# Kernel tuning notes

Hardware: AMD Instinct MI355X
Metric: run time of the kernel (lower is better)

The kernel has to match this reference:

```python
import jax, jax.numpy as jnp
import numpy as np

C = 20        # class_num
B = 2         # boxes per cell, N = B*5 + C = 30
S = 7         # grid size
NB = 16384    # batch
LAMBDA_COORD = 5.0
LAMBDA_NOOBJ = 0.5
OBJ_P = 0.2


def setup_inputs() -> dict:
    key = jax.random.key(0)
    ks = jax.random.split(key, 8)
    pred = jax.random.uniform(ks[0], (NB, S, S, B * 5 + C), jnp.float32)
    # object indicator per cell (target conf channel must be exactly 1 for obj cells)
    obj = (jax.random.uniform(ks[1], (NB, S, S, 1)) < OBJ_P).astype(jnp.float32)
    parts = []
    for b in range(B):
        xy = jax.random.uniform(ks[2 + 2 * b], (NB, S, S, 2), jnp.float32)
        wh = jax.random.uniform(ks[3 + 2 * b], (NB, S, S, 2), jnp.float32) * 0.9 + 0.05
        parts += [xy, wh, obj]
    cls = jax.random.uniform(ks[6], (NB, S, S, C), jnp.float32)
    target = jnp.concatenate(parts + [cls], axis=-1)
    return {"pred_tensor": pred, "target_tensor": target}


def _yolo_loss(pred, target):
    Nb, Sg, _, N = pred.shape
    Bb = (N - C) // 5
    dt = pred.dtype
    # grid[..., 0] = column (x offset), grid[..., 1] = row (y offset)
    gx, gy = jnp.meshgrid(jnp.arange(Sg), jnp.arange(Sg), indexing="xy")
    grid = jnp.stack([gx, gy], axis=-1).astype(dt)          # [S,S,2]

    pb = pred[..., : 5 * Bb].reshape(Nb, Sg, Sg, Bb, 5)      # raw pred boxes [Nb,S,S,B,5]
    tb0 = target[..., :5]                                    # raw gt box 0  [Nb,S,S,5]

    # txty -> absolute xy (normalized by S); wh stays raw
    pxy = (pb[..., :2] + grid[None, :, :, None, :]) / Sg
    pwh = pb[..., 2:4]
    gxy = (tb0[..., :2] + grid[None]) / Sg
    gwh = tb0[..., 2:4]

    # corners
    p1, p2 = pxy - 0.5 * pwh, pxy + 0.5 * pwh                # [Nb,S,S,B,2]
    g1 = (gxy - 0.5 * gwh)[..., None, :]                     # [Nb,S,S,1,2]
    g2 = (gxy + 0.5 * gwh)[..., None, :]

    # IoU of gt box against each of the B pred boxes, per cell
    wh = jnp.clip(jnp.minimum(g2, p2) - jnp.maximum(g1, p1), 0.0)
    inter = wh[..., 0] * wh[..., 1]                          # [Nb,S,S,B]
    area_p = pwh[..., 0] * pwh[..., 1]
    area_g = (gwh[..., 0] * gwh[..., 1])[..., None]
    iou = inter / (area_g + area_p - inter)

    best = jnp.argmax(iou, axis=-1)                          # [Nb,S,S]
    best_iou = jax.lax.stop_gradient(jnp.max(iou, axis=-1))  # .item() in torch detaches
    best_box = jnp.take_along_axis(pb, best[..., None, None], axis=3)[..., 0, :]  # raw [Nb,S,S,5]

    obj = target[..., 4] == 1.0
    objf = obj.astype(dt)
    noobjf = (target[..., 4] < 1.0).astype(dt)

    # coord losses (responsible box only)
    loss_xy = LAMBDA_COORD * jnp.sum(objf[..., None] * (best_box[..., :2] - tb0[..., :2]) ** 2)
    gwh_safe = jnp.where(obj[..., None], gwh, 1.0)           # keep sqrt grads finite under mask
    pwh_safe = jnp.where(obj[..., None], jnp.clip(best_box[..., 2:4], 0.0, 1.0), 1.0)
    loss_wh = LAMBDA_COORD * jnp.sum(objf[..., None] * (jnp.sqrt(pwh_safe) - jnp.sqrt(gwh_safe)) ** 2)

    loss_conf_posi = jnp.sum(objf * (best_box[..., 4] - best_iou) ** 2)
    loss_class = jnp.sum(objf[..., None] * (pred[..., 5 * Bb:] - target[..., 5 * Bb:]) ** 2)

    # negative conf: all B confs in no-obj cells + non-best confs in obj cells
    conf_all = pb[..., 4]                                    # [Nb,S,S,B]
    onehot = jax.nn.one_hot(best, Bb, dtype=dt)
    neg_w = objf[..., None] * (1.0 - onehot) + noobjf[..., None]
    loss_conf_nega = LAMBDA_NOOBJ * jnp.sum(neg_w * conf_all ** 2)

    total = loss_xy + loss_wh + loss_conf_posi + loss_conf_nega + loss_class
    bs = jnp.asarray(Nb, dt)
    return total / bs / bs  # original divides by batch_size twice


def reference(pred_tensor, target_tensor):
    return _yolo_loss(pred_tensor, target_tensor)
```

## Files before the change

kernel.cpp:

```cpp
#include <hip/hip_runtime.h>
#include <math.h>

constexpr int NCH = 30;
constexpr int CPB = 256;
constexpr int NT  = 256;
constexpr int NCHK = CPB * NCH / 4;
constexpr int SPP = 11;
constexpr int STP = 6;

__global__ __launch_bounds__(NT) void yolo_loss_main(
    const float* __restrict__ pred, const float* __restrict__ targ,
    float* __restrict__ partial, int ncells)
{
  __shared__ float sp_box[CPB * SPP];
  __shared__ float st_box[CPB * STP];
  __shared__ float scp[NCHK];
  __shared__ float swred[NT / 64];

  const int tid = threadIdx.x;
  const int cell0 = blockIdx.x * CPB;
  const int nc = min(CPB, ncells - cell0);
  const size_t base = (size_t)cell0 * NCH;

  float sum = 0.0f;

  if (nc == CPB) {
    const float4* gp = (const float4*)(pred + base);
    const float4* gt = (const float4*)(targ + base);
    for (int f = tid; f < NCHK; f += NT) {
      float4 pv = gp[f];
      float4 tv = gt[f];
      int d0 = 4 * f;
      int cell = d0 / NCH;
      int ch0 = d0 - cell * NCH;
      float cp = 0.0f;
      #pragma unroll
      for (int j = 0; j < 4; ++j) {
        int ch = ch0 + j;
        int c = cell;
        if (ch >= NCH) { ch -= NCH; c += 1; }
        float pd = ((const float*)&pv)[j];
        float td = ((const float*)&tv)[j];
        if (ch >= 10) {
          float dd = pd - td;
          cp += dd * dd;
        } else {
          sp_box[c * SPP + ch] = pd;
          if (ch < 5) st_box[c * STP + ch] = td;
        }
      }
      scp[f] = cp;
    }
  } else {
    for (int i = tid; i < NCHK; i += NT) scp[i] = 0.0f;
    for (int i = tid; i < nc; i += NT) {
      const float* p = pred + base + (size_t)i * NCH;
      const float* t = targ + base + (size_t)i * NCH;
      for (int k = 0; k < 10; ++k) sp_box[i * SPP + k] = p[k];
      for (int k = 0; k < 5;  ++k) st_box[i * STP + k] = t[k];
      float o = (t[4] == 1.0f) ? 1.0f : 0.0f;
      for (int k = 10; k < NCH; ++k) {
        float dd = p[k] - t[k];
        sum += o * dd * dd;
      }
    }
  }
  __syncthreads();

  if (tid < nc) {
    const float* p = sp_box + tid * SPP;
    const float* t = st_box + tid * STP;
    int cellg = cell0 + tid;
    int rem = cellg % 49;
    int row = rem / 7;
    float fi = (float)row;
    float fj = (float)(rem - row * 7);

    float tx = t[0], ty = t[1], tw = t[2], th = t[3];
    bool obj = (t[4] == 1.0f);

    if (obj) {
      int m = tid >> 1;
      const float* cpp = scp + 15 * m;
      float cl;
      if ((tid & 1) == 0)
        cl = cpp[2] + cpp[3] + cpp[4] + cpp[5] + cpp[6] + cpp[7];
      else
        cl = cpp[10] + cpp[11] + cpp[12] + cpp[13] + cpp[14];
      sum += cl;
    }

    float gx = (tx + fj) / 7.0f;
    float gy = (ty + fi) / 7.0f;
    float g1x = gx - 0.5f * tw, g1y = gy - 0.5f * th;
    float g2x = gx + 0.5f * tw, g2y = gy + 0.5f * th;
    float area_g = tw * th;

    float px0 = p[0], py0 = p[1], pw0 = p[2], ph0 = p[3], pc0 = p[4];
    float px1 = p[5], py1 = p[6], pw1 = p[7], ph1 = p[8], pc1 = p[9];

    float iou0, iou1;
    {
      float cx = (px0 + fj) / 7.0f, cy = (py0 + fi) / 7.0f;
      float wx = fminf(g2x, cx + 0.5f * pw0) - fmaxf(g1x, cx - 0.5f * pw0);
      float wy = fminf(g2y, cy + 0.5f * ph0) - fmaxf(g1y, cy - 0.5f * ph0);
      wx = fmaxf(wx, 0.0f); wy = fmaxf(wy, 0.0f);
      float inter = wx * wy;
      iou0 = inter / (area_g + pw0 * ph0 - inter);
    }
    {
      float cx = (px1 + fj) / 7.0f, cy = (py1 + fi) / 7.0f;
      float wx = fminf(g2x, cx + 0.5f * pw1) - fmaxf(g1x, cx - 0.5f * pw1);
      float wy = fminf(g2y, cy + 0.5f * ph1) - fmaxf(g1y, cy - 0.5f * ph1);
      wx = fmaxf(wx, 0.0f); wy = fmaxf(wy, 0.0f);
      float inter = wx * wy;
      iou1 = inter / (area_g + pw1 * ph1 - inter);
    }

    bool b1 = (iou1 > iou0);
    float biou = fmaxf(iou0, iou1);

    float lneg = 0.0f;
    if (!obj || b1)  lneg += pc0 * pc0;
    if (!obj || !b1) lneg += pc1 * pc1;
    sum += 0.5f * lneg;

    if (obj) {
      float bx = b1 ? px1 : px0;
      float by = b1 ? py1 : py0;
      float bw = b1 ? pw1 : pw0;
      float bh = b1 ? ph1 : ph0;
      float bc = b1 ? pc1 : pc0;
      float dx = bx - tx, dy = by - ty;
      sum += 5.0f * (dx * dx + dy * dy);
      float cw  = fminf(fmaxf(bw, 0.0f), 1.0f);
      float chh = fminf(fmaxf(bh, 0.0f), 1.0f);
      float sw_ = sqrtf(cw)  - sqrtf(tw);
      float sh_ = sqrtf(chh) - sqrtf(th);
      sum += 5.0f * (sw_ * sw_ + sh_ * sh_);
      float dc = bc - biou;
      sum += dc * dc;
    }
  }

  #pragma unroll
  for (int off = 32; off > 0; off >>= 1) sum += __shfl_down(sum, off);
  if ((tid & 63) == 0) swred[tid >> 6] = sum;
  __syncthreads();
  if (tid == 0) {
    float s = 0.0f;
    #pragma unroll
    for (int w = 0; w < NT / 64; ++w) s += swred[w];
    partial[blockIdx.x] = s;
  }
}

__global__ __launch_bounds__(256) void yolo_loss_reduce(
    const float* __restrict__ partial, int n, float* __restrict__ out,
    float scale)
{
  __shared__ float swred[4];
  float s = 0.0f;
  for (int i = threadIdx.x; i < n; i += 256) s += partial[i];
  #pragma unroll
  for (int off = 32; off > 0; off >>= 1) s += __shfl_down(s, off);
  if ((threadIdx.x & 63) == 0) swred[threadIdx.x >> 6] = s;
  __syncthreads();
  if (threadIdx.x == 0)
    out[0] = (swred[0] + swred[1] + swred[2] + swred[3]) * scale;
}

extern "C" void kernel_launch(void* const* d_in, const int* in_sizes, int n_in,
                              void* d_out, int out_size, void* d_ws, size_t ws_size,
                              hipStream_t stream) {
  const float* pred = (const float*)d_in[0];
  const float* targ = (const float*)d_in[1];
  float* out = (float*)d_out;
  float* partial = (float*)d_ws;

  int total = in_sizes[0];
  int ncells = total / NCH;
  int nb = ncells / 49;
  int blocks = (ncells + CPB - 1) / CPB;
  float scale = 1.0f / ((float)nb * (float)nb);

  yolo_loss_main<<<blocks, NT, 0, stream>>>(pred, targ, partial, ncells);
  yolo_loss_reduce<<<1, 256, 0, stream>>>(partial, blocks, out, scale);
}
```

Baseline: 42.05 us.

## Stage box fields as float4 in LDS and batch global loads per thread

Moves to 320 threads so the 1920 float4 chunks of a 256-cell tile split evenly into six per thread. The chunks are loaded in two unrolled batches of three pred and three target float4s to raise memory-level parallelism. Box fields go into shared memory as whole float4 chunks arranged by cell pair instead of scattered scalar stores, and the compute phase reads them back with float4 LDS loads. This cuts LDS store count and branch divergence but adds register pressure, and 64 of the 320 threads sit idle during the per-cell compute phase.

```diff
diff --git a/kernel.cpp b/kernel.cpp
--- a/kernel.cpp
+++ b/kernel.cpp
@@ -1,21 +1,21 @@
 #include <hip/hip_runtime.h>
 #include <math.h>
 
-constexpr int NCH = 30;
-constexpr int CPB = 256;
-constexpr int NT  = 256;
+constexpr int NCH  = 30;
+constexpr int CPB  = 256;
+constexpr int NT   = 320;
 constexpr int NCHK = CPB * NCH / 4;
-constexpr int SPP = 11;
-constexpr int STP = 6;
+constexpr int NIT  = NCHK / NT;
+
 
 __global__ __launch_bounds__(NT) void yolo_loss_main(
     const float* __restrict__ pred, const float* __restrict__ targ,
     float* __restrict__ partial, int ncells)
 {
-  __shared__ float sp_box[CPB * SPP];
-  __shared__ float st_box[CPB * STP];
-  __shared__ float scp[NCHK];
-  __shared__ float swred[NT / 64];
+  __shared__ float4 sp4[(CPB / 2) * 6];
+  __shared__ float4 st4[(CPB / 2) * 4];
+  __shared__ float  scp[NCHK];
+  __shared__ float  swred[NT / 64];
 
   const int tid = threadIdx.x;
   const int cell0 = blockIdx.x * CPB;
@@ -27,77 +27,120 @@
   if (nc == CPB) {
     const float4* gp = (const float4*)(pred + base);
     const float4* gt = (const float4*)(targ + base);
-    for (int f = tid; f < NCHK; f += NT) {
-      float4 pv = gp[f];
-      float4 tv = gt[f];
-      int d0 = 4 * f;
-      int cell = d0 / NCH;
-      int ch0 = d0 - cell * NCH;
-      float cp = 0.0f;
+
+    #pragma unroll
+    for (int b = 0; b < 2; ++b) {
+      float4 pv[3], tv[3];
       #pragma unroll
-      for (int j = 0; j < 4; ++j) {
-        int ch = ch0 + j;
-        int c = cell;
-        if (ch >= NCH) { ch -= NCH; c += 1; }
-        float pd = ((const float*)&pv)[j];
-        float td = ((const float*)&tv)[j];
-        if (ch >= 10) {
-          float dd = pd - td;
-          cp += dd * dd;
-        } else {
-          sp_box[c * SPP + ch] = pd;
-          if (ch < 5) st_box[c * STP + ch] = td;
+      for (int i = 0; i < 3; ++i) pv[i] = gp[(3 * b + i) * NT + tid];
+      #pragma unroll
+      for (int i = 0; i < 3; ++i) tv[i] = gt[(3 * b + i) * NT + tid];
+
+      #pragma unroll
+      for (int i = 0; i < 3; ++i) {
+        int f = (3 * b + i) * NT + tid;
+        int m = f / 15;
+        int k = f - m * 15;
+        int ch0 = 4 * k - (k >= 8 ? 30 : 0);
+
+        float cp = 0.0f;
+        #pragma unroll
+        for (int j = 0; j < 4; ++j) {
+          int ch = ch0 + j;
+          bool cls = (ch >= 10) & (ch < 30);
+          float d = ((const float*)&pv[i])[j] - ((const float*)&tv[i])[j];
+          cp += cls ? d * d : 0.0f;
+        }
+        scp[f] = cp;
+
+        if (k < 3 || (k >= 7 && k <= 9)) {
+          int ps = (k < 3) ? k : (k - 4);
+          sp4[m * 6 + ps] = pv[i];
+        }
+        if (k < 2 || k == 7 || k == 8) {
+          int ts = (k < 2) ? k : (k - 5);
+          st4[m * 4 + ts] = tv[i];
         }
       }
-      scp[f] = cp;
     }
   } else {
     for (int i = tid; i < NCHK; i += NT) scp[i] = 0.0f;
+    float* spf = (float*)sp4;
+    float* stf = (float*)st4;
     for (int i = tid; i < nc; i += NT) {
       const float* p = pred + base + (size_t)i * NCH;
       const float* t = targ + base + (size_t)i * NCH;
-      for (int k = 0; k < 10; ++k) sp_box[i * SPP + k] = p[k];
-      for (int k = 0; k < 5;  ++k) st_box[i * STP + k] = t[k];
+      int m = i >> 1;
+      if ((i & 1) == 0) {
+        for (int q = 0; q < 8; ++q) spf[(m * 6 + 0) * 4 + q] = p[q];
+        spf[(m * 6 + 2) * 4 + 0] = p[8];
+        spf[(m * 6 + 2) * 4 + 1] = p[9];
+        for (int q = 0; q < 4; ++q) stf[(m * 4 + 0) * 4 + q] = t[q];
+        stf[(m * 4 + 1) * 4 + 0] = t[4];
+      } else {
+        spf[(m * 6 + 3) * 4 + 2] = p[0];
+        spf[(m * 6 + 3) * 4 + 3] = p[1];
+        for (int q = 0; q < 8; ++q) spf[(m * 6 + 4) * 4 + q] = p[2 + q];
+        stf[(m * 4 + 2) * 4 + 2] = t[0];
+        stf[(m * 4 + 2) * 4 + 3] = t[1];
+        stf[(m * 4 + 3) * 4 + 0] = t[2];
+        stf[(m * 4 + 3) * 4 + 1] = t[3];
+        stf[(m * 4 + 3) * 4 + 2] = t[4];
+      }
       float o = (t[4] == 1.0f) ? 1.0f : 0.0f;
-      for (int k = 10; k < NCH; ++k) {
-        float dd = p[k] - t[k];
-        sum += o * dd * dd;
-      }
+      float cs = 0.0f;
+      for (int q = 10; q < NCH; ++q) { float d = p[q] - t[q]; cs += d * d; }
+      sum += o * cs;
     }
   }
   __syncthreads();
 
   if (tid < nc) {
-    const float* p = sp_box + tid * SPP;
-    const float* t = st_box + tid * STP;
+    int m = tid >> 1;
+    bool odd = tid & 1;
+    float4 A = sp4[m * 6 + (odd ? 3 : 0)];
+    float4 B = sp4[m * 6 + (odd ? 4 : 1)];
+    float4 Cc = sp4[m * 6 + (odd ? 5 : 2)];
+    float px0, py0, pw0, ph0, pc0, px1, py1, pw1, ph1, pc1;
+    float tx, ty, tw, th, tobj;
+    if (!odd) {
+      px0 = A.x;  py0 = A.y;  pw0 = A.z;  ph0 = A.w;
+      pc0 = B.x;  px1 = B.y;  py1 = B.z;  pw1 = B.w;
+      ph1 = Cc.x; pc1 = Cc.y;
+      float4 T0 = st4[m * 4 + 0];
+      tx = T0.x; ty = T0.y; tw = T0.z; th = T0.w;
+      tobj = st4[m * 4 + 1].x;
+    } else {
+      px0 = A.z;  py0 = A.w;
+      pw0 = B.x;  ph0 = B.y;  pc0 = B.z;  px1 = B.w;
+      py1 = Cc.x; pw1 = Cc.y; ph1 = Cc.z; pc1 = Cc.w;
+      float4 T2 = st4[m * 4 + 2];
+      float4 T3 = st4[m * 4 + 3];
+      tx = T2.z; ty = T2.w; tw = T3.x; th = T3.y; tobj = T3.z;
+    }
+    bool obj = (tobj == 1.0f);
+
+    if (obj) {
+      const float* cpp = scp + 15 * m;
+      float cl;
+      if (!odd)
+        cl = cpp[2] + cpp[3] + cpp[4] + cpp[5] + cpp[6] + cpp[7];
+      else
+        cl = cpp[10] + cpp[11] + cpp[12] + cpp[13] + cpp[14];
+      sum += cl;
+    }
+
     int cellg = cell0 + tid;
     int rem = cellg % 49;
     int row = rem / 7;
     float fi = (float)row;
     float fj = (float)(rem - row * 7);
 
-    float tx = t[0], ty = t[1], tw = t[2], th = t[3];
-    bool obj = (t[4] == 1.0f);
-
-    if (obj) {
-      int m = tid >> 1;
-      const float* cpp = scp + 15 * m;
-      float cl;
-      if ((tid & 1) == 0)
-        cl = cpp[2] + cpp[3] + cpp[4] + cpp[5] + cpp[6] + cpp[7];
-      else
-        cl = cpp[10] + cpp[11] + cpp[12] + cpp[13] + cpp[14];
-      sum += cl;
-    }
-
     float gx = (tx + fj) / 7.0f;
     float gy = (ty + fi) / 7.0f;
     float g1x = gx - 0.5f * tw, g1y = gy - 0.5f * th;
     float g2x = gx + 0.5f * tw, g2y = gy + 0.5f * th;
     float area_g = tw * th;
-
-    float px0 = p[0], py0 = p[1], pw0 = p[2], ph0 = p[3], pc0 = p[4];
-    float px1 = p[5], py1 = p[6], pw1 = p[7], ph1 = p[8], pc1 = p[9];
 
     float iou0, iou1;
     {
```

Result: faster. 39.00 us (median of 2 runs) (-7.3%).
